# Performance work log

Measured on AMD Instinct MI355X. Metric: run time of the kernel, lower is better.

Reference implementation:

```python
import jax, jax.numpy as jnp
import numpy as np

N_NODES = 110
C = 4096  # in_channels = hidden = out_channels


def setup_inputs() -> dict:
    key = jax.random.key(0)
    ks = jax.random.split(key, 8)
    x = jax.random.normal(ks[0], (N_NODES, C), dtype=jnp.float32)
    adj = jax.random.randint(ks[1], (N_NODES, N_NODES), 0, 2, dtype=jnp.int32)
    # torch.nn.Linear weights stored [out_features, in_features]
    W2 = jax.random.normal(ks[2], (C, C), dtype=jnp.float32) / np.sqrt(C)
    b2 = jax.random.normal(ks[3], (C,), dtype=jnp.float32) * 0.01
    W1 = jax.random.normal(ks[4], (2 * C, C), dtype=jnp.float32) / np.sqrt(2 * C)
    b1 = jax.random.normal(ks[5], (C,), dtype=jnp.float32) * 0.01
    Wl = jax.random.normal(ks[6], (N_NODES, N_NODES), dtype=jnp.float32) / np.sqrt(N_NODES)
    bl = jax.random.normal(ks[7], (N_NODES,), dtype=jnp.float32) * 0.01
    # note: W1 is stored [in=2C, out=C]; W2 [in=C, out=C]; Wl [in=110, out=110]
    return {"x": x, "adj": adj, "W2": W2, "b2": b2, "W1": W1, "b1": b1, "Wl": Wl, "bl": bl}


def reference(x, adj, W2, b2, W1, b1, Wl, bl):
    # FeatGraphConv: h = lin2(x)
    h = x @ W2 + b2  # [N, C]
    # edge_index.nonzero(): adjacency -> edge list (i=src, j=dst); mean-aggregate
    # h[src] at dst. Dense equivalent: column-normalized mask matmul.
    mask = (adj != 0).astype(x.dtype)  # [N, N]
    deg = mask.sum(axis=0)  # in-degree of each target node j
    aggr = (mask.T @ h) / jnp.maximum(deg, 1.0)[:, None]  # [N, C]; 0 for isolated nodes (PyG mean)
    # update: lin1(cat(h, aggr)) then relu (in RegGNN.forward)
    out = jax.nn.relu(jnp.concatenate([h, aggr], axis=1) @ W1 + b1)  # [N, C]
    # x.t(); lin(110,110); x.t()
    out = (out.T @ Wl.T + bl).T  # [N, C]
    return out
```

## Files before the change

### kernel.cpp

```cpp
#include <hip/hip_runtime.h>
#include <hip/hip_fp16.h>

#define C 4096
#define NN 110
#define NMT 7
#define KBS (NMT * 512)
#define NSLICE 8

typedef _Float16 f16x8 __attribute__((ext_vector_type(8)));
typedef float fx4 __attribute__((ext_vector_type(4)));
typedef unsigned long long ull;

__device__ __forceinline__ size_t fragidx(int n, int c) {
    return (size_t)(c >> 5) * KBS + (n >> 4) * 512
         + (((c >> 3) & 3) * 16 + (n & 15)) * 8 + (c & 7);
}

__global__ __launch_bounds__(256)
void prep1_kernel(const float* __restrict__ x, _Float16* __restrict__ A1t,
                  const int* __restrict__ adj, ull* __restrict__ mlo,
                  ull* __restrict__ mhi, float* __restrict__ degs) {
    if (blockIdx.x == 224) {
        int j = threadIdx.x;
        if (j < NN) {
            ull lo = 0, hi = 0; int dg = 0;
            for (int i = 0; i < 64; ++i) {
                int m = (adj[i * NN + j] != 0);
                lo |= ((ull)m) << i; dg += m;
            }
            for (int i = 64; i < NN; ++i) {
                int m = (adj[i * NN + j] != 0);
                hi |= ((ull)m) << (i - 64); dg += m;
            }
            mlo[j] = lo; mhi[j] = hi;
            degs[j] = (float)(dg > 0 ? dg : 1);
        }
        return;
    }
    int u = blockIdx.x * 256 + threadIdx.x;
    int kb  = u / 448;
    int rem = u - kb * 448;
    int mt  = rem >> 6;
    int L   = rem & 63;
    int n   = mt * 16 + (L & 15);
    int c   = kb * 32 + (L >> 4) * 8;
    f16x8 hv;
    if (n < NN) {
        float4 v0 = *(const float4*)(x + (size_t)n * C + c);
        float4 v1 = *(const float4*)(x + (size_t)n * C + c + 4);
        hv[0]=(_Float16)v0.x; hv[1]=(_Float16)v0.y; hv[2]=(_Float16)v0.z; hv[3]=(_Float16)v0.w;
        hv[4]=(_Float16)v1.x; hv[5]=(_Float16)v1.y; hv[6]=(_Float16)v1.z; hv[7]=(_Float16)v1.w;
    } else {
        for (int e = 0; e < 8; ++e) hv[e] = (_Float16)0.f;
    }
    *(f16x8*)(A1t + (size_t)u * 8) = hv;
}

template<int NITER>
__global__ __launch_bounds__(256, 2)
void mm_kernel(const _Float16* __restrict__ A, const float* __restrict__ B,
               float* __restrict__ Cpart) {
    const int t   = threadIdx.x;
    const int j0  = blockIdx.x * 64;
    const int y   = blockIdx.y;
    const int w   = t >> 6;
    const int L   = t & 63;
    const int l15 = L & 15;
    const int q   = L >> 4;
    const int qq8 = q * 8;

    fx4 acc[7];
#pragma unroll
    for (int mt = 0; mt < 7; ++mt) acc[mt] = (fx4){0.f, 0.f, 0.f, 0.f};

    const _Float16* ApL  = A + (size_t)y * (NITER * 2) * KBS + L * 8;
    const float*    Bcol = B + (size_t)y * (NITER * 64) * C + j0 + w * 16 + l15;

    f16x8 af[2][2][7];
    float bw[2][2][8];

#define LOADAF(buf, ch)                                                        \
    { _Pragma("unroll")                                                        \
      for (int s = 0; s < 2; ++s)                                              \
          _Pragma("unroll")                                                    \
          for (int mt = 0; mt < 7; ++mt)                                       \
              af[buf][s][mt] = *(const f16x8*)(ApL                             \
                  + (size_t)((ch) * 2 + s) * KBS + mt * 512); }

#define LOADBW(buf, ch)                                                        \
    { _Pragma("unroll")                                                        \
      for (int s = 0; s < 2; ++s)                                              \
          _Pragma("unroll")                                                    \
          for (int e = 0; e < 8; ++e)                                          \
              bw[buf][s][e] =                                                  \
                  Bcol[(size_t)((ch) * 64 + s * 32 + qq8 + e) * C]; }

    LOADAF(0, 0);
    LOADBW(0, 0);

#pragma unroll
    for (int it = 0; it < NITER; ++it) {
        if (it + 1 < NITER) {
            LOADAF((it + 1) & 1, it + 1);
            LOADBW((it + 1) & 1, it + 1);
        }
#pragma unroll
        for (int s = 0; s < 2; ++s) {
            f16x8 bf;
#pragma unroll
            for (int e = 0; e < 8; ++e) bf[e] = (_Float16)bw[it & 1][s][e];
#pragma unroll
            for (int mt = 0; mt < 7; ++mt)
                acc[mt] = __builtin_amdgcn_mfma_f32_16x16x32_f16(
                    af[it & 1][s][mt], bf, acc[mt], 0, 0, 0);
        }
    }

    float* Cp = Cpart + (size_t)y * (NN * C) + j0 + w * 16 + l15;
#pragma unroll
    for (int mt = 0; mt < 7; ++mt)
#pragma unroll
        for (int r = 0; r < 4; ++r) {
            int row = mt * 16 + q * 4 + r;
            if (row < NN)
                Cp[(size_t)row * C] = acc[mt][r];
        }
#undef LOADAF
#undef LOADBW
}

__global__ __launch_bounds__(256)
void agg_kernel(const float* __restrict__ hpart, const ull* __restrict__ gmlo,
                const ull* __restrict__ gmhi, const float* __restrict__ gdegs,
                const float* __restrict__ b2, _Float16* __restrict__ A3t) {
    __shared__ float hb[NN * 16];
    const int t  = threadIdx.x;
    const int c0 = blockIdx.x * 16;

    for (int idx = t; idx < NN * 8; idx += 256) {
        int n = idx >> 3, cp = (idx & 7) << 1;
        float v0 = b2[c0 + cp], v1 = b2[c0 + cp + 1];
#pragma unroll
        for (int p = 0; p < NSLICE; ++p) {
            float2 v = *(const float2*)(hpart + (size_t)p * (NN * C)
                                        + (size_t)n * C + c0 + cp);
            v0 += v.x; v1 += v.y;
        }
        hb[n * 16 + cp]     = v0;
        hb[n * 16 + cp + 1] = v1;
        union { _Float16 h[2]; unsigned u; } pk;
        pk.h[0] = (_Float16)v0;
        pk.h[1] = (_Float16)v1;
        *(unsigned*)(A3t + fragidx(n, c0 + cp)) = pk.u;
    }
    if (t < 32) {
        int n  = 110 + ((t >> 3) & 1);
        int hs = t >> 4;
        int cp = (t & 7) << 1;
        *(unsigned*)(A3t + fragidx(n, hs * C + c0 + cp)) = 0u;
    }
    __syncthreads();
    for (int idx = t; idx < NN * 8; idx += 256) {
        int j = idx >> 3, cp = (idx & 7) << 1;
        ull lo = gmlo[j], hi = gmhi[j];
        float dg = gdegs[j];
        float a0 = 0.f, a1 = 0.f;
        for (int i = 0; i < 64; ++i)
            if ((lo >> i) & 1) { a0 += hb[i * 16 + cp]; a1 += hb[i * 16 + cp + 1]; }
        for (int i = 64; i < NN; ++i)
            if ((hi >> (i - 64)) & 1) { a0 += hb[i * 16 + cp]; a1 += hb[i * 16 + cp + 1]; }
        union { _Float16 h[2]; unsigned u; } pk;
        pk.h[0] = (_Float16)(a0 / dg);
        pk.h[1] = (_Float16)(a1 / dg);
        *(unsigned*)(A3t + fragidx(j, C + c0 + cp)) = pk.u;
    }
}

__global__ __launch_bounds__(256)
void zred_kernel(const float* __restrict__ zpart, float* __restrict__ z_raw) {
    int idx = blockIdx.x * 256 + threadIdx.x;
    if (idx < NN * (C / 4)) {
        fx4 s = (fx4){0.f, 0.f, 0.f, 0.f};
#pragma unroll
        for (int p = 0; p < NSLICE; ++p) {
            fx4 v = *(const fx4*)(zpart + (size_t)p * (NN * C) + (size_t)idx * 4);
            s.x += v.x; s.y += v.y; s.z += v.z; s.w += v.w;
        }
        *(fx4*)(z_raw + (size_t)idx * 4) = s;
    }
}

__global__ __launch_bounds__(256)
void fin_kernel(const float* __restrict__ z_raw, const float* __restrict__ b1,
                const float* __restrict__ Wl, const float* __restrict__ bl,
                float* __restrict__ out) {
    __shared__ float zs[NN * 64];
    const int t  = threadIdx.x;
    const int c0 = blockIdx.x * 64;
    const int c  = t & 63;

    for (int idx = t; idx < NN * 64; idx += 256) {
        int k = idx >> 6, cc = idx & 63;
        float v = z_raw[(size_t)k * C + c0 + cc] + b1[c0 + cc];
        zs[idx] = fmaxf(v, 0.f);
    }
    __syncthreads();
    for (int jj = 0; jj < 7; ++jj) {
        int j = blockIdx.y * 28 + jj * 4 + (t >> 6);
        if (j < NN) {
            float a = bl[j];
#pragma unroll 2
            for (int k = 0; k < NN; ++k)
                a += Wl[j * NN + k] * zs[k * 64 + c];
            out[(size_t)j * C + c0 + c] = a;
        }
    }
}

extern "C" void kernel_launch(void* const* d_in, const int* in_sizes, int n_in,
                              void* d_out, int out_size, void* d_ws, size_t ws_size,
                              hipStream_t stream) {
    const float* x   = (const float*)d_in[0];
    const int*   adj = (const int*)d_in[1];
    const float* W2  = (const float*)d_in[2];
    const float* b2  = (const float*)d_in[3];
    const float* W1  = (const float*)d_in[4];
    const float* b1  = (const float*)d_in[5];
    const float* Wl  = (const float*)d_in[6];
    const float* bl  = (const float*)d_in[7];
    float* out = (float*)d_out;

    char* ws = (char*)d_ws;
    float*    hpart = (float*)(ws);
    float*    zpart = (float*)(ws + 14417920);
    float*    z_raw = (float*)(ws + 28835840);
    _Float16* A1t   = (_Float16*)(ws + 30638080);
    _Float16* A3t   = (_Float16*)(ws + 31555584);
    ull*      mlo   = (ull*)(ws + 33390592);
    ull*      mhi   = (ull*)(ws + 33391472);
    float*    degs  = (float*)(ws + 33392352);

    prep1_kernel<<<225, 256, 0, stream>>>(x, A1t, adj, mlo, mhi, degs);
    mm_kernel<8><<<dim3(64, NSLICE), 256, 0, stream>>>(A1t, W2, hpart);
    agg_kernel<<<C / 16, 256, 0, stream>>>(hpart, mlo, mhi, degs, b2, A3t);
    mm_kernel<16><<<dim3(64, NSLICE), 256, 0, stream>>>(A3t, W1, zpart);
    zred_kernel<<<440, 256, 0, stream>>>(zpart, z_raw);
    fin_kernel<<<dim3(C / 64, 4), 256, 0, stream>>>(z_raw, b1, Wl, bl, out);
}
```

Baseline: 361.5 us.

## Pre-pack W1/W2 into fp16 MFMA fragment layout before the GEMMs

Adds a pack kernel that converts the fp32 weight matrices W2 and W1 to fp16 and stores them in the exact fragment order the MFMA B operand wants. The x conversion and adjacency mask work are merged into the same launch. The GEMM kernels then load one contiguous 16-byte vector per fragment instead of eight strided fp32 loads plus an in-loop conversion. The goal is to cut latency-bound strided loads in the main GEMMs and spread the conversion over many more blocks. The cost is extra memory traffic each call: the weights are read once in fp32, written in fp16, then read again.

Measured after the change: 404.1 us. 1.12x slower.

```diff
diff --git a/kernel.cpp b/kernel.cpp
--- a/kernel.cpp
+++ b/kernel.cpp
@@ -17,67 +17,91 @@
 }
 
 __global__ __launch_bounds__(256)
-void prep1_kernel(const float* __restrict__ x, _Float16* __restrict__ A1t,
-                  const int* __restrict__ adj, ull* __restrict__ mlo,
-                  ull* __restrict__ mhi, float* __restrict__ degs) {
-    if (blockIdx.x == 224) {
-        int j = threadIdx.x;
-        if (j < NN) {
-            ull lo = 0, hi = 0; int dg = 0;
-            for (int i = 0; i < 64; ++i) {
-                int m = (adj[i * NN + j] != 0);
-                lo |= ((ull)m) << i; dg += m;
-            }
-            for (int i = 64; i < NN; ++i) {
-                int m = (adj[i * NN + j] != 0);
-                hi |= ((ull)m) << (i - 64); dg += m;
-            }
-            mlo[j] = lo; mhi[j] = hi;
-            degs[j] = (float)(dg > 0 ? dg : 1);
-        }
+void pack_kernel(const float* __restrict__ W2, const float* __restrict__ W1,
+                 const float* __restrict__ x, const int* __restrict__ adj,
+                 _Float16* __restrict__ Bpk1, _Float16* __restrict__ Bpk2,
+                 _Float16* __restrict__ A1t, ull* __restrict__ mlo,
+                 ull* __restrict__ mhi, float* __restrict__ degs) {
+    const int bid = blockIdx.x;
+    const int t   = threadIdx.x;
+
+    if (bid < 24576) {
+        const float* W;
+        _Float16*    O;
+        int jb, kc;
+        if (bid < 8192) { W = W2; O = Bpk1; jb = bid >> 7; kc = bid & 127; }
+        else { int ti = bid - 8192; W = W1; O = Bpk2; jb = ti >> 8; kc = ti & 255; }
+        const int w   = t >> 6;
+        const int L   = t & 63;
+        const int q   = L >> 4;
+        const int l15 = L & 15;
+        const float* src = W + (size_t)(kc * 32 + q * 8) * C + jb * 64 + w * 16 + l15;
+        f16x8 hv;
+#pragma unroll
+        for (int e = 0; e < 8; ++e)
+            hv[e] = (_Float16)src[(size_t)e * C];
+        *(f16x8*)(O + ((size_t)(jb << (bid < 8192 ? 7 : 8)) + kc) * 2048
+                  + w * 512 + L * 8) = hv;
         return;
     }
-    int u = blockIdx.x * 256 + threadIdx.x;
-    int kb  = u / 448;
-    int rem = u - kb * 448;
-    int mt  = rem >> 6;
-    int L   = rem & 63;
-    int n   = mt * 16 + (L & 15);
-    int c   = kb * 32 + (L >> 4) * 8;
-    f16x8 hv;
-    if (n < NN) {
-        float4 v0 = *(const float4*)(x + (size_t)n * C + c);
-        float4 v1 = *(const float4*)(x + (size_t)n * C + c + 4);
-        hv[0]=(_Float16)v0.x; hv[1]=(_Float16)v0.y; hv[2]=(_Float16)v0.z; hv[3]=(_Float16)v0.w;
-        hv[4]=(_Float16)v1.x; hv[5]=(_Float16)v1.y; hv[6]=(_Float16)v1.z; hv[7]=(_Float16)v1.w;
-    } else {
-        for (int e = 0; e < 8; ++e) hv[e] = (_Float16)0.f;
-    }
-    *(f16x8*)(A1t + (size_t)u * 8) = hv;
-}
-
-template<int NITER>
+    if (bid < 24800) {
+        int u   = (bid - 24576) * 256 + t;
+        int kb  = u / 448;
+        int rem = u - kb * 448;
+        int mt  = rem >> 6;
+        int L   = rem & 63;
+        int n   = mt * 16 + (L & 15);
+        int c   = kb * 32 + (L >> 4) * 8;
+        f16x8 hv;
+        if (n < NN) {
+            float4 v0 = *(const float4*)(x + (size_t)n * C + c);
+            float4 v1 = *(const float4*)(x + (size_t)n * C + c + 4);
+            hv[0]=(_Float16)v0.x; hv[1]=(_Float16)v0.y; hv[2]=(_Float16)v0.z; hv[3]=(_Float16)v0.w;
+            hv[4]=(_Float16)v1.x; hv[5]=(_Float16)v1.y; hv[6]=(_Float16)v1.z; hv[7]=(_Float16)v1.w;
+        } else {
+            for (int e = 0; e < 8; ++e) hv[e] = (_Float16)0.f;
+        }
+        *(f16x8*)(A1t + (size_t)u * 8) = hv;
+        return;
+    }
+    int j = t;
+    if (j < NN) {
+        ull lo = 0, hi = 0; int dg = 0;
+        for (int i = 0; i < 64; ++i) {
+            int m = (adj[i * NN + j] != 0);
+            lo |= ((ull)m) << i; dg += m;
+        }
+        for (int i = 64; i < NN; ++i) {
+            int m = (adj[i * NN + j] != 0);
+            hi |= ((ull)m) << (i - 64); dg += m;
+        }
+        mlo[j] = lo; mhi[j] = hi;
+        degs[j] = (float)(dg > 0 ? dg : 1);
+    }
+}
+
+template<int NITER, int KC>
 __global__ __launch_bounds__(256, 2)
-void mm_kernel(const _Float16* __restrict__ A, const float* __restrict__ B,
+void mm_kernel(const _Float16* __restrict__ A, const _Float16* __restrict__ Bpk,
                float* __restrict__ Cpart) {
     const int t   = threadIdx.x;
-    const int j0  = blockIdx.x * 64;
+    const int jb  = blockIdx.x;
     const int y   = blockIdx.y;
     const int w   = t >> 6;
     const int L   = t & 63;
     const int l15 = L & 15;
     const int q   = L >> 4;
-    const int qq8 = q * 8;
 
     fx4 acc[7];
 #pragma unroll
     for (int mt = 0; mt < 7; ++mt) acc[mt] = (fx4){0.f, 0.f, 0.f, 0.f};
 
-    const _Float16* ApL  = A + (size_t)y * (NITER * 2) * KBS + L * 8;
-    const float*    Bcol = B + (size_t)y * (NITER * 64) * C + j0 + w * 16 + l15;
+    const _Float16* ApL = A + (size_t)y * (NITER * 2) * KBS + L * 8;
+    const _Float16* BpL = Bpk + ((size_t)jb * KC + y * (NITER * 2)) * 2048
+                        + w * 512 + L * 8;
 
     f16x8 af[2][2][7];
-    float bw[2][2][8];
+    f16x8 bf[2][2];
 
 #define LOADAF(buf, ch)                                                        \
     { _Pragma("unroll")                                                        \
@@ -87,36 +111,29 @@
               af[buf][s][mt] = *(const f16x8*)(ApL                             \
                   + (size_t)((ch) * 2 + s) * KBS + mt * 512); }
 
-#define LOADBW(buf, ch)                                                        \
+#define LOADBF(buf, ch)                                                        \
     { _Pragma("unroll")                                                        \
       for (int s = 0; s < 2; ++s)                                              \
-          _Pragma("unroll")                                                    \
-          for (int e = 0; e < 8; ++e)                                          \
-              bw[buf][s][e] =                                                  \
-                  Bcol[(size_t)((ch) * 64 + s * 32 + qq8 + e) * C]; }
+          bf[buf][s] = *(const f16x8*)(BpL + (size_t)((ch) * 2 + s) * 2048); }
 
     LOADAF(0, 0);
-    LOADBW(0, 0);
+    LOADBF(0, 0);
 
 #pragma unroll
     for (int it = 0; it < NITER; ++it) {
         if (it + 1 < NITER) {
             LOADAF((it + 1) & 1, it + 1);
-            LOADBW((it + 1) & 1, it + 1);
-        }
-#pragma unroll
-        for (int s = 0; s < 2; ++s) {
-            f16x8 bf;
-#pragma unroll
-            for (int e = 0; e < 8; ++e) bf[e] = (_Float16)bw[it & 1][s][e];
+            LOADBF((it + 1) & 1, it + 1);
+        }
+#pragma unroll
+        for (int s = 0; s < 2; ++s)
 #pragma unroll
             for (int mt = 0; mt < 7; ++mt)
                 acc[mt] = __builtin_amdgcn_mfma_f32_16x16x32_f16(
-                    af[it & 1][s][mt], bf, acc[mt], 0, 0, 0);
-        }
-    }
-
-    float* Cp = Cpart + (size_t)y * (NN * C) + j0 + w * 16 + l15;
+                    af[it & 1][s][mt], bf[it & 1][s], acc[mt], 0, 0, 0);
+    }
+
+    float* Cp = Cpart + (size_t)y * (NN * C) + jb * 64 + w * 16 + l15;
 #pragma unroll
     for (int mt = 0; mt < 7; ++mt)
 #pragma unroll
@@ -126,7 +143,7 @@
                 Cp[(size_t)row * C] = acc[mt][r];
         }
 #undef LOADAF
-#undef LOADBW
+#undef LOADBF
 }
 
 __global__ __launch_bounds__(256)
@@ -239,11 +256,14 @@
     ull*      mlo   = (ull*)(ws + 33390592);
     ull*      mhi   = (ull*)(ws + 33391472);
     float*    degs  = (float*)(ws + 33392352);
-
-    prep1_kernel<<<225, 256, 0, stream>>>(x, A1t, adj, mlo, mhi, degs);
-    mm_kernel<8><<<dim3(64, NSLICE), 256, 0, stream>>>(A1t, W2, hpart);
+    _Float16* Bpk1  = (_Float16*)(ws + 33554432);
+    _Float16* Bpk2  = (_Float16*)(ws + 67108864);
+
+    pack_kernel<<<24801, 256, 0, stream>>>(W2, W1, x, adj, Bpk1, Bpk2,
+                                           A1t, mlo, mhi, degs);
+    mm_kernel<8, 128><<<dim3(64, NSLICE), 256, 0, stream>>>(A1t, Bpk1, hpart);
     agg_kernel<<<C / 16, 256, 0, stream>>>(hpart, mlo, mhi, degs, b2, A3t);
-    mm_kernel<16><<<dim3(64, NSLICE), 256, 0, stream>>>(A3t, W1, zpart);
+    mm_kernel<16, 256><<<dim3(64, NSLICE), 256, 0, stream>>>(A3t, Bpk2, zpart);
     zred_kernel<<<440, 256, 0, stream>>>(zpart, z_raw);
     fin_kernel<<<dim3(C / 64, 4), 256, 0, stream>>>(z_raw, b1, Wl, bl, out);
 }
```

## Stage B tiles through LDS with direct global-to-LDS loads, triple-buffered

Applied to the files above, without the earlier changes.

The GEMM kernel used to read B (fp32 weights) with strided scalar global loads into registers. It now copies each 64x64 B chunk into shared memory with global_load_lds 16-byte transfers, triple-buffered and prefetched two chunks ahead. Fragments are then read from LDS, synchronised with explicit vmcnt waits and barriers. This aims for coalesced wide loads and lower register pressure, at the cost of 48KB of LDS per block, which may limit occupancy, and fragile hand-counted waitcnt values.

Measured after the change: 352.4 us. 1.03x faster.

```diff
diff --git a/kernel.cpp b/kernel.cpp
--- a/kernel.cpp
+++ b/kernel.cpp
@@ -14,6 +14,12 @@
 __device__ __forceinline__ size_t fragidx(int n, int c) {
     return (size_t)(c >> 5) * KBS + (n >> 4) * 512
          + (((c >> 3) & 3) * 16 + (n & 15)) * 8 + (c & 7);
+}
+
+__device__ __forceinline__ void glds16(const float* g, float* l) {
+    __builtin_amdgcn_global_load_lds(
+        (const __attribute__((address_space(1))) void*)g,
+        (__attribute__((address_space(3))) void*)l, 16, 0, 0);
 }
 
 __global__ __launch_bounds__(256)
@@ -56,10 +62,12 @@
     *(f16x8*)(A1t + (size_t)u * 8) = hv;
 }
 
-template<int NITER>
+template<int NC>
 __global__ __launch_bounds__(256, 2)
 void mm_kernel(const _Float16* __restrict__ A, const float* __restrict__ B,
                float* __restrict__ Cpart) {
+    __shared__ __align__(16) float Bs[3][64 * 64];
+
     const int t   = threadIdx.x;
     const int j0  = blockIdx.x * 64;
     const int y   = blockIdx.y;
@@ -67,17 +75,22 @@
     const int L   = t & 63;
     const int l15 = L & 15;
     const int q   = L >> 4;
-    const int qq8 = q * 8;
 
     fx4 acc[7];
 #pragma unroll
     for (int mt = 0; mt < 7; ++mt) acc[mt] = (fx4){0.f, 0.f, 0.f, 0.f};
 
-    const _Float16* ApL  = A + (size_t)y * (NITER * 2) * KBS + L * 8;
-    const float*    Bcol = B + (size_t)y * (NITER * 64) * C + j0 + w * 16 + l15;
+    const float*    gB  = B + (size_t)(y * NC * 64 + w * 16 + (L >> 4)) * C
+                        + j0 + (L & 15) * 4;
+    const _Float16* ApL = A + (size_t)(y * NC * 2) * KBS + L * 8;
 
     f16x8 af[2][2][7];
-    float bw[2][2][8];
+
+#define GLDS(ch, bufi)                                                         \
+    { _Pragma("unroll")                                                        \
+      for (int i = 0; i < 4; ++i)                                              \
+          glds16(gB + (size_t)((ch) * 64 + i * 4) * C,                         \
+                 &Bs[bufi][(w * 16 + i * 4) * 64]); }
 
 #define LOADAF(buf, ch)                                                        \
     { _Pragma("unroll")                                                        \
@@ -87,32 +100,35 @@
               af[buf][s][mt] = *(const f16x8*)(ApL                             \
                   + (size_t)((ch) * 2 + s) * KBS + mt * 512); }
 
-#define LOADBW(buf, ch)                                                        \
-    { _Pragma("unroll")                                                        \
-      for (int s = 0; s < 2; ++s)                                              \
-          _Pragma("unroll")                                                    \
-          for (int e = 0; e < 8; ++e)                                          \
-              bw[buf][s][e] =                                                  \
-                  Bcol[(size_t)((ch) * 64 + s * 32 + qq8 + e) * C]; }
-
+    GLDS(0, 0);
+    GLDS(1, 1);
     LOADAF(0, 0);
-    LOADBW(0, 0);
-
-#pragma unroll
-    for (int it = 0; it < NITER; ++it) {
-        if (it + 1 < NITER) {
-            LOADAF((it + 1) & 1, it + 1);
-            LOADBW((it + 1) & 1, it + 1);
-        }
+    asm volatile("s_waitcnt vmcnt(18)" ::: "memory");
+    __builtin_amdgcn_sched_barrier(0);
+    __builtin_amdgcn_s_barrier();
+    __builtin_amdgcn_sched_barrier(0);
+
+#pragma unroll
+    for (int it = 0; it < NC; ++it) {
+        if (it + 2 < NC) GLDS(it + 2, (it + 2) % 3);
+        if (it + 1 < NC) LOADAF((it + 1) & 1, it + 1);
+        __builtin_amdgcn_sched_barrier(0);
 #pragma unroll
         for (int s = 0; s < 2; ++s) {
+            const float* bp = &Bs[it % 3][(s * 32 + q * 8) * 64 + w * 16 + l15];
             f16x8 bf;
 #pragma unroll
-            for (int e = 0; e < 8; ++e) bf[e] = (_Float16)bw[it & 1][s][e];
+            for (int e = 0; e < 8; ++e) bf[e] = (_Float16)bp[e * 64];
 #pragma unroll
             for (int mt = 0; mt < 7; ++mt)
                 acc[mt] = __builtin_amdgcn_mfma_f32_16x16x32_f16(
                     af[it & 1][s][mt], bf, acc[mt], 0, 0, 0);
+        }
+        if (it + 1 < NC) {
+            asm volatile("s_waitcnt vmcnt(18)" ::: "memory");
+            __builtin_amdgcn_sched_barrier(0);
+            __builtin_amdgcn_s_barrier();
+            __builtin_amdgcn_sched_barrier(0);
         }
     }
 
@@ -125,8 +141,8 @@
             if (row < NN)
                 Cp[(size_t)row * C] = acc[mt][r];
         }
+#undef GLDS
 #undef LOADAF
-#undef LOADBW
 }
 
 __global__ __launch_bounds__(256)
```
